# Kernel optimization log

Measured on AMD Instinct MI355X. Metric: run time of the kernel, lower is better.

Reference implementation:

```python
import jax, jax.numpy as jnp
import numpy as np

E = 8192      # number of original edges -> artificial nodes
N = 2048      # number of original graph nodes (id range)
C_IN = 128
C_OUT = 128
NEG_SLOPE = 0.2


def setup_inputs() -> dict:
    key = jax.random.key(0)
    k1, k2, k3, k4, k5 = jax.random.split(key, 5)
    x = jax.random.normal(k1, (E, C_IN), dtype=jnp.float32)
    edge_index = jax.random.randint(k2, (2, E), 0, N, dtype=jnp.int64)
    # GATConv params (heads=1): linear weight, attention vectors, bias
    W = jax.random.normal(k3, (C_IN, C_OUT), dtype=jnp.float32) / np.sqrt(C_IN)
    att_src = jax.random.normal(k4, (C_OUT,), dtype=jnp.float32) / np.sqrt(C_OUT)
    att_dst = jax.random.normal(k5, (C_OUT,), dtype=jnp.float32) / np.sqrt(C_OUT)
    bias = jnp.zeros((C_OUT,), dtype=jnp.float32)
    return {"x": x, "edge_index": edge_index, "W": W,
            "att_src": att_src, "att_dst": att_dst, "bias": bias}


def reference(x, edge_index, W, att_src, att_dst, bias):
    # --- line-graph construction (vectorized version of the O(E^2) loop) ---
    s = edge_index[0]  # [E] source node of each original edge
    d = edge_index[1]  # [E] target node of each original edge
    share = ((s[:, None] == s[None, :]) | (s[:, None] == d[None, :]) |
             (d[:, None] == s[None, :]) | (d[:, None] == d[None, :]))  # [E,E]
    eye = jnp.eye(x.shape[0], dtype=bool)
    # original loop only adds pairs i != j (symmetrically); GATConv then adds self loops
    adj = (share & ~eye) | eye  # adj[i, j]: message j -> i allowed

    # --- GATConv (heads=1, concat) over the dense line-graph adjacency ---
    h = x @ W                       # [E, C_OUT]
    a_src = h @ att_src             # [E] per-source attention logit
    a_dst = h @ att_dst             # [E] per-target attention logit
    scores = a_dst[:, None] + a_src[None, :]          # [E,E], row=target, col=source
    scores = jax.nn.leaky_relu(scores, NEG_SLOPE)
    scores = jnp.where(adj, scores, -jnp.inf)
    alpha = jax.nn.softmax(scores, axis=1)            # softmax over source edges per target
    out = alpha @ h + bias          # [E, C_OUT]
    return out
```

## Files before the change

kernel.cpp:

```cpp
#include <hip/hip_runtime.h>

#define E 8192
#define NNODE 2048
#define C 128
#define CAPN 32
#define RPB 16
#define NGEMM (E / RPB)

typedef unsigned int u32;
typedef unsigned long long u64;

__global__ __launch_bounds__(256) void gat_prep(
    const float* __restrict__ x, const float* __restrict__ W,
    const float* __restrict__ att_s, const float* __restrict__ att_d,
    const float* __restrict__ bias, const int* __restrict__ ei,
    float* __restrict__ h, float* __restrict__ asrc, float* __restrict__ adst,
    int* __restrict__ packed, int* __restrict__ cnt, int* __restrict__ nlist)
{
    const int tid = threadIdx.x, lane = tid & 63, wv = tid >> 6;
    const int g = blockIdx.x * 256 + tid;
    if (g < E) {
        const int s = ei[g], d = ei[E + g];
        packed[g] = (s << 16) | d;
        int slot = atomicAdd(&cnt[s], 1);
        if (slot < CAPN) nlist[s * CAPN + slot] = g;
        if (d != s) {
            slot = atomicAdd(&cnt[d], 1);
            if (slot < CAPN) nlist[d * CAPN + slot] = g;
        }
    }

    __shared__ __align__(16) float xs[RPB * C];
    const int row0 = (int)blockIdx.x * RPB;
    {
        const float4* xg = reinterpret_cast<const float4*>(x + (size_t)row0 * C);
        float4* xsv = reinterpret_cast<float4*>(xs);
        xsv[tid]       = xg[tid];
        xsv[tid + 256] = xg[tid + 256];
    }
    __syncthreads();

    float a0x = 0.f, a0y = 0.f, a1x = 0.f, a1y = 0.f;
    float a2x = 0.f, a2y = 0.f, a3x = 0.f, a3y = 0.f;
    const float4* xp0 = reinterpret_cast<const float4*>(xs + (wv * 4 + 0) * C);
    const float4* xp1 = reinterpret_cast<const float4*>(xs + (wv * 4 + 1) * C);
    const float4* xp2 = reinterpret_cast<const float4*>(xs + (wv * 4 + 2) * C);
    const float4* xp3 = reinterpret_cast<const float4*>(xs + (wv * 4 + 3) * C);
    const float* Wc = W + 2 * lane;

#define ROWFMA(V, AX, AY)                                    \
    AX = fmaf(V.x, w0.x, AX); AY = fmaf(V.x, w0.y, AY);      \
    AX = fmaf(V.y, w1.x, AX); AY = fmaf(V.y, w1.y, AY);      \
    AX = fmaf(V.z, w2.x, AX); AY = fmaf(V.z, w2.y, AY);      \
    AX = fmaf(V.w, w3.x, AX); AY = fmaf(V.w, w3.y, AY);
    for (int k4 = 0; k4 < C / 4; ++k4) {
        const float4 v0 = xp0[k4], v1 = xp1[k4], v2 = xp2[k4], v3 = xp3[k4];
        const float2 w0 = *reinterpret_cast<const float2*>(Wc + (4 * k4 + 0) * C);
        const float2 w1 = *reinterpret_cast<const float2*>(Wc + (4 * k4 + 1) * C);
        const float2 w2 = *reinterpret_cast<const float2*>(Wc + (4 * k4 + 2) * C);
        const float2 w3 = *reinterpret_cast<const float2*>(Wc + (4 * k4 + 3) * C);
        ROWFMA(v0, a0x, a0y) ROWFMA(v1, a1x, a1y)
        ROWFMA(v2, a2x, a2y) ROWFMA(v3, a3x, a3y)
    }
#undef ROWFMA

    const float2 asv = *reinterpret_cast<const float2*>(att_s + 2 * lane);
    const float2 adv = *reinterpret_cast<const float2*>(att_d + 2 * lane);
    const float2 bv  = *reinterpret_cast<const float2*>(bias  + 2 * lane);
    const int rw0 = row0 + wv * 4;
#define EPI(R, AX, AY) {                                                        \
    *reinterpret_cast<float2*>(&h[(size_t)(rw0 + R) * C + 2 * lane]) =          \
        make_float2(AX + bv.x, AY + bv.y);              \
    float ps = fmaf(AX, asv.x, AY * asv.y);                                     \
    float pd = fmaf(AX, adv.x, AY * adv.y);                                     \
    _Pragma("unroll")                                                           \
    for (int off = 32; off > 0; off >>= 1) {                                    \
        ps += __shfl_xor(ps, off); pd += __shfl_xor(pd, off);                   \
    }                                                                           \
    if (lane == 0) { asrc[rw0 + R] = ps; adst[rw0 + R] = pd; } }
    EPI(0, a0x, a0y) EPI(1, a1x, a1y) EPI(2, a2x, a2y) EPI(3, a3x, a3y)
#undef EPI
}

__global__ __launch_bounds__(256) void gat_aggr(
    const int* __restrict__ packed, const float* __restrict__ h,
    const float* __restrict__ asrc, const float* __restrict__ adst,
    const int* __restrict__ cnt, const int* __restrict__ nlist,
    float* __restrict__ out)
{
    __shared__ float2 lst[4][64];
    const int tid = threadIdx.x, lane = tid & 63, wv = tid >> 6;
    const int i = blockIdx.x * 4 + wv;

    const u32 pi = (u32)packed[i];
    const int si = (int)(pi >> 16), di = (int)(pi & 0xffffu);
    const float adi = adst[i];
    int len_s = cnt[si]; if (len_s > CAPN) len_s = CAPN;
    int len_d = (di == si) ? 0 : cnt[di]; if (len_d > CAPN) len_d = CAPN;
    const int ntot = len_s + len_d;

    int key = 0x7fffffff;
    float sc = -INFINITY;
    bool valid = false;
    if (lane < ntot) {
        const bool from_s = lane < len_s;
        const int j = nlist[(from_s ? si : di) * CAPN + (from_s ? lane : lane - len_s)];
        const u32 pj = (u32)packed[j];
        valid = from_s || ((int)(pj >> 16) != si && (int)(pj & 0xffffu) != si);
        if (valid) {
            const float s0 = adi + asrc[j];
            sc = s0 >= 0.f ? s0 : 0.2f * s0;
            key = j;
        }
    }

    float m = sc;
    #pragma unroll
    for (int off = 32; off > 0; off >>= 1) m = fmaxf(m, __shfl_xor(m, off));
    const int nvalid = (int)__popcll(__ballot(valid));

    float p = __expf(sc - m);

    #pragma unroll
    for (int k = 2; k <= 64; k <<= 1) {
        #pragma unroll
        for (int st = k >> 1; st > 0; st >>= 1) {
            const int   ok = __shfl_xor(key, st);
            const float op = __shfl_xor(p, st);
            const bool takeMin = ((lane & k) == 0) == ((lane & st) == 0);
            if (takeMin ? (ok < key) : (ok > key)) { key = ok; p = op; }
        }
    }
    lst[wv][lane] = make_float2(__int_as_float(key == 0x7fffffff ? i : key), p);

    const int nch = (nvalid + 3) >> 2;
    float lsum = 0.f, o0 = 0.f, o1 = 0.f;
    const float* hb = h + 2 * lane;
    for (int t = 0; t < nch; ++t) {
        const float2 e0 = lst[wv][4 * t + 0];
        const float2 e1 = lst[wv][4 * t + 1];
        const float2 e2 = lst[wv][4 * t + 2];
        const float2 e3 = lst[wv][4 * t + 3];
        const float2 h0 = *reinterpret_cast<const float2*>(hb + (size_t)__float_as_int(e0.x) * C);
        const float2 h1 = *reinterpret_cast<const float2*>(hb + (size_t)__float_as_int(e1.x) * C);
        const float2 h2 = *reinterpret_cast<const float2*>(hb + (size_t)__float_as_int(e2.x) * C);
        const float2 h3 = *reinterpret_cast<const float2*>(hb + (size_t)__float_as_int(e3.x) * C);
        lsum += (e0.y + e1.y) + (e2.y + e3.y);
        o0 = fmaf(e0.y, h0.x, o0); o1 = fmaf(e0.y, h0.y, o1);
        o0 = fmaf(e1.y, h1.x, o0); o1 = fmaf(e1.y, h1.y, o1);
        o0 = fmaf(e2.y, h2.x, o0); o1 = fmaf(e2.y, h2.y, o1);
        o0 = fmaf(e3.y, h3.x, o0); o1 = fmaf(e3.y, h3.y, o1);
    }
    const float inv = 1.0f / lsum;
    *reinterpret_cast<float2*>(&out[(size_t)i * C + 2 * lane]) =
        make_float2(o0 * inv, o1 * inv);
}

extern "C" void kernel_launch(void* const* d_in, const int* in_sizes, int n_in,
                              void* d_out, int out_size, void* d_ws, size_t ws_size,
                              hipStream_t stream) {
    const float* x     = (const float*)d_in[0];
    const int*   ei    = (const int*)d_in[1];
    const float* W     = (const float*)d_in[2];
    const float* att_s = (const float*)d_in[3];
    const float* att_d = (const float*)d_in[4];
    const float* bias  = (const float*)d_in[5];

    float* h      = (float*)d_ws;
    float* asrc   = h + (size_t)E * C;
    float* adst   = asrc + E;
    int*   packed = (int*)(adst + E);
    int*   cnt    = packed + E;
    int*   nlist  = cnt + NNODE;

    hipMemsetAsync(cnt, 0, NNODE * sizeof(int), stream);
    gat_prep<<<NGEMM, 256, 0, stream>>>(x, W, att_s, att_d, bias, ei,
                                        h, asrc, adst, packed, cnt, nlist);
    gat_aggr<<<E / 4, 256, 0, stream>>>(packed, h, asrc, adst, cnt, nlist,
                                        (float*)d_out);
}
```

Before: 43.05 us.

## Fuse prep, adjacency build and aggregation into one cooperative kernel with grid syncs

Merges the memset, the GEMM/prep kernel and the aggregation kernel into a single cooperative launch of 512 blocks. Grid-wide syncs separate counter zeroing, neighbour-list construction and aggregation, and each wave now aggregates four rows in a loop. This removes the memset and one kernel launch, at the cost of two grid barriers and less parallelism in the aggregation phase. The cooperative launch requires all 512 blocks to be co-resident, which the launch bound of 2 blocks per CU is meant to allow.

```diff
diff --git a/kernel.cpp b/kernel.cpp
--- a/kernel.cpp
+++ b/kernel.cpp
@@ -1,37 +1,44 @@
 #include <hip/hip_runtime.h>
+#include <hip/hip_cooperative_groups.h>
+
+namespace cg = cooperative_groups;
 
 #define E 8192
 #define NNODE 2048
 #define C 128
 #define CAPN 32
 #define RPB 16
-#define NGEMM (E / RPB)
+#define NBLK (E / RPB)
 
 typedef unsigned int u32;
 typedef unsigned long long u64;
 
-__global__ __launch_bounds__(256) void gat_prep(
+__global__ __launch_bounds__(256, 2) void gat_fused(
     const float* __restrict__ x, const float* __restrict__ W,
     const float* __restrict__ att_s, const float* __restrict__ att_d,
     const float* __restrict__ bias, const int* __restrict__ ei,
     float* __restrict__ h, float* __restrict__ asrc, float* __restrict__ adst,
-    int* __restrict__ packed, int* __restrict__ cnt, int* __restrict__ nlist)
+    int* __restrict__ packed, int* __restrict__ cnt, int* __restrict__ nlist,
+    float* __restrict__ out)
 {
+    cg::grid_group grid = cg::this_grid();
     const int tid = threadIdx.x, lane = tid & 63, wv = tid >> 6;
-    const int g = blockIdx.x * 256 + tid;
-    if (g < E) {
-        const int s = ei[g], d = ei[E + g];
-        packed[g] = (s << 16) | d;
-        int slot = atomicAdd(&cnt[s], 1);
-        if (slot < CAPN) nlist[s * CAPN + slot] = g;
-        if (d != s) {
-            slot = atomicAdd(&cnt[d], 1);
-            if (slot < CAPN) nlist[d * CAPN + slot] = g;
-        }
-    }
+    const int bid = (int)blockIdx.x;
 
     __shared__ __align__(16) float xs[RPB * C];
-    const int row0 = (int)blockIdx.x * RPB;
+    __shared__ float2 lst[4][64];
+
+    if (bid < NNODE / 256) cnt[bid * 256 + tid] = 0;
+
+    int es = 0, ed = 0;
+    const int g = bid * 256 + tid;
+    const bool has_edge = g < E;
+    if (has_edge) {
+        es = ei[g]; ed = ei[E + g];
+        packed[g] = (es << 16) | ed;
+    }
+
+    const int row0 = bid * RPB;
     {
         const float4* xg = reinterpret_cast<const float4*>(x + (size_t)row0 * C);
         float4* xsv = reinterpret_cast<float4*>(xs);
@@ -64,10 +71,11 @@
     }
 #undef ROWFMA
 
-    const float2 asv = *reinterpret_cast<const float2*>(att_s + 2 * lane);
-    const float2 adv = *reinterpret_cast<const float2*>(att_d + 2 * lane);
-    const float2 bv  = *reinterpret_cast<const float2*>(bias  + 2 * lane);
-    const int rw0 = row0 + wv * 4;
+    {
+        const float2 asv = *reinterpret_cast<const float2*>(att_s + 2 * lane);
+        const float2 adv = *reinterpret_cast<const float2*>(att_d + 2 * lane);
+        const float2 bv  = *reinterpret_cast<const float2*>(bias  + 2 * lane);
+        const int rw0 = row0 + wv * 4;
 #define EPI(R, AX, AY) {                                                        \
     *reinterpret_cast<float2*>(&h[(size_t)(rw0 + R) * C + 2 * lane]) =          \
         make_float2(AX + bv.x, AY + bv.y);              \
@@ -78,82 +86,90 @@
         ps += __shfl_xor(ps, off); pd += __shfl_xor(pd, off);                   \
     }                                                                           \
     if (lane == 0) { asrc[rw0 + R] = ps; adst[rw0 + R] = pd; } }
-    EPI(0, a0x, a0y) EPI(1, a1x, a1y) EPI(2, a2x, a2y) EPI(3, a3x, a3y)
+        EPI(0, a0x, a0y) EPI(1, a1x, a1y) EPI(2, a2x, a2y) EPI(3, a3x, a3y)
 #undef EPI
-}
-
-__global__ __launch_bounds__(256) void gat_aggr(
-    const int* __restrict__ packed, const float* __restrict__ h,
-    const float* __restrict__ asrc, const float* __restrict__ adst,
-    const int* __restrict__ cnt, const int* __restrict__ nlist,
-    float* __restrict__ out)
-{
-    __shared__ float2 lst[4][64];
-    const int tid = threadIdx.x, lane = tid & 63, wv = tid >> 6;
-    const int i = blockIdx.x * 4 + wv;
-
-    const u32 pi = (u32)packed[i];
-    const int si = (int)(pi >> 16), di = (int)(pi & 0xffffu);
-    const float adi = adst[i];
-    int len_s = cnt[si]; if (len_s > CAPN) len_s = CAPN;
-    int len_d = (di == si) ? 0 : cnt[di]; if (len_d > CAPN) len_d = CAPN;
-    const int ntot = len_s + len_d;
-
-    int key = 0x7fffffff;
-    float sc = -INFINITY;
-    bool valid = false;
-    if (lane < ntot) {
-        const bool from_s = lane < len_s;
-        const int j = nlist[(from_s ? si : di) * CAPN + (from_s ? lane : lane - len_s)];
-        const u32 pj = (u32)packed[j];
-        valid = from_s || ((int)(pj >> 16) != si && (int)(pj & 0xffffu) != si);
-        if (valid) {
-            const float s0 = adi + asrc[j];
-            sc = s0 >= 0.f ? s0 : 0.2f * s0;
-            key = j;
-        }
-    }
-
-    float m = sc;
-    #pragma unroll
-    for (int off = 32; off > 0; off >>= 1) m = fmaxf(m, __shfl_xor(m, off));
-    const int nvalid = (int)__popcll(__ballot(valid));
-
-    float p = __expf(sc - m);
-
-    #pragma unroll
-    for (int k = 2; k <= 64; k <<= 1) {
+    }
+
+    grid.sync();
+
+    if (has_edge) {
+        int slot = atomicAdd(&cnt[es], 1);
+        if (slot < CAPN) nlist[es * CAPN + slot] = g;
+        if (ed != es) {
+            slot = atomicAdd(&cnt[ed], 1);
+            if (slot < CAPN) nlist[ed * CAPN + slot] = g;
+        }
+    }
+
+    grid.sync();
+
+    const int wgid = bid * 4 + wv;
+    for (int e4 = 0; e4 < 4; ++e4) {
+        const int i = wgid * 4 + e4;
+
+        const u32 pi = (u32)packed[i];
+        const int si = (int)(pi >> 16), di = (int)(pi & 0xffffu);
+        const float adi = adst[i];
+        int len_s = cnt[si]; if (len_s > CAPN) len_s = CAPN;
+        int len_d = (di == si) ? 0 : cnt[di]; if (len_d > CAPN) len_d = CAPN;
+        const int ntot = len_s + len_d;
+
+        int key = 0x7fffffff;
+        float sc = -INFINITY;
+        bool valid = false;
+        if (lane < ntot) {
+            const bool from_s = lane < len_s;
+            const int j = nlist[(from_s ? si : di) * CAPN + (from_s ? lane : lane - len_s)];
+            const u32 pj = (u32)packed[j];
+            valid = from_s || ((int)(pj >> 16) != si && (int)(pj & 0xffffu) != si);
+            if (valid) {
+                const float s0 = adi + asrc[j];
+                sc = s0 >= 0.f ? s0 : 0.2f * s0;
+                key = j;
+            }
+        }
+
+        float m = sc;
         #pragma unroll
-        for (int st = k >> 1; st > 0; st >>= 1) {
-            const int   ok = __shfl_xor(key, st);
-            const float op = __shfl_xor(p, st);
-            const bool takeMin = ((lane & k) == 0) == ((lane & st) == 0);
-            if (takeMin ? (ok < key) : (ok > key)) { key = ok; p = op; }
-        }
-    }
-    lst[wv][lane] = make_float2(__int_as_float(key == 0x7fffffff ? i : key), p);
-
-    const int nch = (nvalid + 3) >> 2;
-    float lsum = 0.f, o0 = 0.f, o1 = 0.f;
-    const float* hb = h + 2 * lane;
-    for (int t = 0; t < nch; ++t) {
-        const float2 e0 = lst[wv][4 * t + 0];
-        const float2 e1 = lst[wv][4 * t + 1];
-        const float2 e2 = lst[wv][4 * t + 2];
-        const float2 e3 = lst[wv][4 * t + 3];
-        const float2 h0 = *reinterpret_cast<const float2*>(hb + (size_t)__float_as_int(e0.x) * C);
-        const float2 h1 = *reinterpret_cast<const float2*>(hb + (size_t)__float_as_int(e1.x) * C);
-        const float2 h2 = *reinterpret_cast<const float2*>(hb + (size_t)__float_as_int(e2.x) * C);
-        const float2 h3 = *reinterpret_cast<const float2*>(hb + (size_t)__float_as_int(e3.x) * C);
-        lsum += (e0.y + e1.y) + (e2.y + e3.y);
-        o0 = fmaf(e0.y, h0.x, o0); o1 = fmaf(e0.y, h0.y, o1);
-        o0 = fmaf(e1.y, h1.x, o0); o1 = fmaf(e1.y, h1.y, o1);
-        o0 = fmaf(e2.y, h2.x, o0); o1 = fmaf(e2.y, h2.y, o1);
-        o0 = fmaf(e3.y, h3.x, o0); o1 = fmaf(e3.y, h3.y, o1);
-    }
-    const float inv = 1.0f / lsum;
-    *reinterpret_cast<float2*>(&out[(size_t)i * C + 2 * lane]) =
-        make_float2(o0 * inv, o1 * inv);
+        for (int off = 32; off > 0; off >>= 1) m = fmaxf(m, __shfl_xor(m, off));
+        const int nvalid = (int)__popcll(__ballot(valid));
+
+        float p = __expf(sc - m);
+
+        #pragma unroll
+        for (int k = 2; k <= 64; k <<= 1) {
+            #pragma unroll
+            for (int st = k >> 1; st > 0; st >>= 1) {
+                const int   ok = __shfl_xor(key, st);
+                const float op = __shfl_xor(p, st);
+                const bool takeMin = ((lane & k) == 0) == ((lane & st) == 0);
+                if (takeMin ? (ok < key) : (ok > key)) { key = ok; p = op; }
+            }
+        }
+        lst[wv][lane] = make_float2(__int_as_float(key == 0x7fffffff ? i : key), p);
+
+        const int nch = (nvalid + 3) >> 2;
+        float lsum = 0.f, o0 = 0.f, o1 = 0.f;
+        const float* hb = h + 2 * lane;
+        for (int t = 0; t < nch; ++t) {
+            const float2 e0 = lst[wv][4 * t + 0];
+            const float2 e1 = lst[wv][4 * t + 1];
+            const float2 e2 = lst[wv][4 * t + 2];
+            const float2 e3 = lst[wv][4 * t + 3];
+            const float2 h0 = *reinterpret_cast<const float2*>(hb + (size_t)__float_as_int(e0.x) * C);
+            const float2 h1 = *reinterpret_cast<const float2*>(hb + (size_t)__float_as_int(e1.x) * C);
+            const float2 h2 = *reinterpret_cast<const float2*>(hb + (size_t)__float_as_int(e2.x) * C);
+            const float2 h3 = *reinterpret_cast<const float2*>(hb + (size_t)__float_as_int(e3.x) * C);
+            lsum += (e0.y + e1.y) + (e2.y + e3.y);
+            o0 = fmaf(e0.y, h0.x, o0); o1 = fmaf(e0.y, h0.y, o1);
+            o0 = fmaf(e1.y, h1.x, o0); o1 = fmaf(e1.y, h1.y, o1);
+            o0 = fmaf(e2.y, h2.x, o0); o1 = fmaf(e2.y, h2.y, o1);
+            o0 = fmaf(e3.y, h3.x, o0); o1 = fmaf(e3.y, h3.y, o1);
+        }
+        const float inv = 1.0f / lsum;
+        *reinterpret_cast<float2*>(&out[(size_t)i * C + 2 * lane]) =
+            make_float2(o0 * inv, o1 * inv);
+    }
 }
 
 extern "C" void kernel_launch(void* const* d_in, const int* in_sizes, int n_in,
@@ -172,10 +188,17 @@
     int*   packed = (int*)(adst + E);
     int*   cnt    = packed + E;
     int*   nlist  = cnt + NNODE;
-
-    hipMemsetAsync(cnt, 0, NNODE * sizeof(int), stream);
-    gat_prep<<<NGEMM, 256, 0, stream>>>(x, W, att_s, att_d, bias, ei,
-                                        h, asrc, adst, packed, cnt, nlist);
-    gat_aggr<<<E / 4, 256, 0, stream>>>(packed, h, asrc, adst, cnt, nlist,
-                                        (float*)d_out);
+    float* out    = (float*)d_out;
+
+    void* args[13];
+    args[0]  = (void*)&x;      args[1]  = (void*)&W;
+    args[2]  = (void*)&att_s;  args[3]  = (void*)&att_d;
+    args[4]  = (void*)&bias;   args[5]  = (void*)&ei;
+    args[6]  = (void*)&h;      args[7]  = (void*)&asrc;
+    args[8]  = (void*)&adst;   args[9]  = (void*)&packed;
+    args[10] = (void*)&cnt;    args[11] = (void*)&nlist;
+    args[12] = (void*)&out;
+
+    hipLaunchCooperativeKernel((const void*)gat_fused, dim3(NBLK), dim3(256),
+                               args, 0, stream);
 }
```

New measurement: 152.4 us. 254% more time.
